# Kernel optimization log

Measured on AMD Instinct MI355X. Metric: run time of the kernel, lower is better.

Reference implementation:

```python
import jax, jax.numpy as jnp
import numpy as np

N_NODES = 100000
N_EDGES = 1600000
D_NODE = 32
D_EDGE = 16
D_HID = 64
D_OUT = 32


def setup_inputs() -> dict:
    key = jax.random.key(0)
    ks = jax.random.split(key, 7)
    x = jax.random.normal(ks[0], (N_NODES, D_NODE), dtype=jnp.float32)
    edge_index = jax.random.randint(ks[1], (2, N_EDGES), 0, N_NODES, dtype=jnp.int64)
    edge_attr = jax.random.normal(ks[2], (N_EDGES, D_EDGE), dtype=jnp.float32)
    # 2-layer MLP params (Linear -> ReLU -> Linear), He-ish scaling
    W1 = jax.random.normal(ks[3], (D_NODE + D_EDGE, D_HID), dtype=jnp.float32) * (2.0 / (D_NODE + D_EDGE)) ** 0.5
    b1 = jnp.zeros((D_HID,), dtype=jnp.float32)
    W2 = jax.random.normal(ks[4], (D_HID, D_OUT), dtype=jnp.float32) * (2.0 / D_HID) ** 0.5
    b2 = jnp.zeros((D_OUT,), dtype=jnp.float32)
    return {"x": x, "edge_index": edge_index, "edge_attr": edge_attr,
            "W1": W1, "b1": b1, "W2": W2, "b2": b2}


def reference(x, edge_index, edge_attr, W1, b1, W2, b2):
    row, col = edge_index[0], edge_index[1]
    # gather source-node feats and concat with edge feats: [E, d_node + d_edge]
    inp = jnp.concatenate([x[col], edge_attr], axis=1)
    # 2-layer MLP over edges
    h = jax.nn.relu(inp @ W1 + b1)
    messages = h @ W2 + b2  # [E, d_out]
    # scatter-sum aggregate by destination node
    message = jax.ops.segment_sum(messages, row, num_segments=x.shape[0])
    return message
```

## Files before the change

### kernel.cpp

```cpp
#include <hip/hip_runtime.h>
#include <hip/hip_bf16.h>
#include <stdint.h>

#define N_NODES 100000
#define N_EDGES 1600000
#define D_NODE  32
#define D_EDGE  16
#define D_IN    48
#define D_HID   64
#define D_OUT   32

#define NFLAGS_OFF  ((size_t)0)
#define NB1_OFF     ((size_t)64)
#define NB2_OFF     ((size_t)320)
#define W1BF_OFF    ((size_t)1024)
#define W2BF_OFF    ((size_t)9216)
#define COUNTS_OFF  ((size_t)65536)
#define OFFSETS_OFF ((size_t)466944)
#define BLKSUM_OFF  ((size_t)917504)
#define RANK_OFF    ((size_t)1048576)
#define MSG_OFF     ((size_t)8388608)

#define SCAN_NB 391

typedef __attribute__((ext_vector_type(8))) short bf16x8;
typedef __attribute__((ext_vector_type(4))) float f32x4;

__device__ inline float bf2f(unsigned int u16) {
    return __uint_as_float(u16 << 16);
}
__device__ inline unsigned short f2bf_rne(float f) {
    unsigned int x = __float_as_uint(f);
    unsigned int r = (x + 0x7FFFu + ((x >> 16) & 1u)) >> 16;
    return (unsigned short)r;
}
__device__ inline unsigned int pk_bf2(float a, float b) {
    float2 f; f.x = a; f.y = b;
    __hip_bfloat162 h = __float22bfloat162_rn(f);
    return *reinterpret_cast<unsigned int*>(&h);
}
__device__ inline float ld_f(const void* p, int i, int isbf) {
    if (isbf) return bf2f(((const unsigned short*)p)[i]);
    return ((const float*)p)[i];
}
__device__ inline bf16x8 pack_bf8(float4 v0, float4 v1) {
    union { unsigned int u[4]; bf16x8 v; } r;
    r.u[0] = pk_bf2(v0.x, v0.y);
    r.u[1] = pk_bf2(v0.z, v0.w);
    r.u[2] = pk_bf2(v1.x, v1.y);
    r.u[3] = pk_bf2(v1.z, v1.w);
    return r.v;
}

__global__ void prep_kernel(const void* __restrict__ xq, const void* __restrict__ idxq,
                            const void* __restrict__ W1q, const void* __restrict__ b1q,
                            const void* __restrict__ W2q, const void* __restrict__ b2q,
                            char* __restrict__ ws) {
    __shared__ int s_isbf;
    const int t = threadIdx.x;
    if (t < 64) {
        unsigned short u = ((const unsigned short*)xq)[t];
        unsigned long long mb = __ballot(((u >> 7) & 0xFF) >= 140);
        int wodd = ((const int*)idxq)[2 * t + 1];
        unsigned long long mi = __ballot(wodd != 0);
        if (t == 0) {
            int* flags = (int*)(ws + NFLAGS_OFF);
            flags[0] = (mb == 0ULL);
            flags[1] = (mi == 0ULL);
            s_isbf = (mb == 0ULL);
        }
    }
    __syncthreads();
    const int isbf = s_isbf;
    float* b1 = (float*)(ws + NB1_OFF);
    float* b2 = (float*)(ws + NB2_OFF);
    unsigned short* w1b = (unsigned short*)(ws + W1BF_OFF);
    unsigned short* w2b = (unsigned short*)(ws + W2BF_OFF);

    if (t < D_HID) b1[t] = ld_f(b1q, t, isbf);
    if (t < D_OUT) b2[t] = ld_f(b2q, t, isbf);

    for (int i = t; i < D_HID * 64; i += blockDim.x) {
        int n = i >> 6, k = i & 63;
        float v = (k < D_IN) ? ld_f(W1q, k * D_HID + n, isbf) : 0.0f;
        w1b[i] = f2bf_rne(v);
    }
    for (int i = t; i < D_OUT * 64; i += blockDim.x) {
        int n = i >> 6, k = i & 63;
        w2b[i] = f2bf_rne(ld_f(W2q, k * D_OUT + n, isbf));
    }
}

__global__ __launch_bounds__(256) void hist_kernel(const void* __restrict__ idxq,
                                                   char* __restrict__ ws,
                                                   int* __restrict__ rankb) {
    const int is64 = ((const int*)(ws + NFLAGS_OFF))[1];
    const int e = blockIdx.x * 256 + threadIdx.x;
    int dst;
    if (is64) dst = (int)((const long long*)idxq)[e];
    else      dst = ((const int*)idxq)[e];
    rankb[e] = atomicAdd((int*)(ws + COUNTS_OFF) + dst, 1);
}

__global__ __launch_bounds__(256) void scan_block_kernel(char* __restrict__ ws) {
    __shared__ int s[256];
    const int* counts = (const int*)(ws + COUNTS_OFF);
    int* offs   = (int*)(ws + OFFSETS_OFF);
    int* blksum = (int*)(ws + BLKSUM_OFF);
    const int t = threadIdx.x;
    const int i = blockIdx.x * 256 + t;
    int v = (i < N_NODES) ? counts[i] : 0;
    s[t] = v;
    __syncthreads();
    for (int d = 1; d < 256; d <<= 1) {
        int a = (t >= d) ? s[t - d] : 0;
        __syncthreads();
        s[t] += a;
        __syncthreads();
    }
    if (i < N_NODES) offs[i] = s[t] - v;
    if (t == 255) blksum[blockIdx.x] = s[255];
}

__global__ __launch_bounds__(256) void scan_add_kernel(char* __restrict__ ws) {
    __shared__ int s[256];
    int* offs = (int*)(ws + OFFSETS_OFF);
    const int* blksum = (const int*)(ws + BLKSUM_OFF);
    const int t = threadIdx.x;
    const int b = blockIdx.x;
    int acc = 0;
    for (int j = t; j < b; j += 256) acc += blksum[j];
    s[t] = acc;
    __syncthreads();
    for (int d = 128; d > 0; d >>= 1) {
        if (t < d) s[t] += s[t + d];
        __syncthreads();
    }
    const int prefix = s[0];
    const int i = b * 256 + t;
    if (i < N_NODES) offs[i] += prefix;
    if (i == 0) offs[N_NODES] = N_EDGES;
}

__global__ __launch_bounds__(64) void edge_mlp_mfma_kernel(
        const void* __restrict__ xq,
        const void* __restrict__ idxq,
        const void* __restrict__ eaq,
        const char* __restrict__ wsro,
        const int* __restrict__ rankb,
        unsigned short* __restrict__ msg) {
    const int isbf = ((const int*)(wsro + NFLAGS_OFF))[0];
    const int is64 = ((const int*)(wsro + NFLAGS_OFF))[1];

    __shared__ __align__(16) unsigned short hbuf[2][16][72];

    const int l   = threadIdx.x;
    const int m16 = l & 15;
    const int q   = l >> 4;

    const unsigned short* w1b = (const unsigned short*)(wsro + W1BF_OFF);
    const unsigned short* w2b = (const unsigned short*)(wsro + W2BF_OFF);
    const float* b1 = (const float*)(wsro + NB1_OFF);
    const float* b2 = (const float*)(wsro + NB2_OFF);
    const int* offs = (const int*)(wsro + OFFSETS_OFF);

    bf16x8 w1f[4][2], w2f[2][2];
#pragma unroll
    for (int t = 0; t < 4; ++t)
#pragma unroll
        for (int c = 0; c < 2; ++c)
            w1f[t][c] = *(const bf16x8*)(w1b + ((t * 16 + m16) * 64 + c * 32 + q * 8));
#pragma unroll
    for (int t = 0; t < 2; ++t)
#pragma unroll
        for (int c = 0; c < 2; ++c)
            w2f[t][c] = *(const bf16x8*)(w2b + ((t * 16 + m16) * 64 + c * 32 + q * 8));

    const int eb = blockIdx.x * 64;

    int srcv[4], posv[4];
#pragma unroll
    for (int g = 0; g < 4; ++g) {
        const int e = eb + g * 16 + m16;
        int dst;
        if (is64) {
            const long long* ip = (const long long*)idxq;
            dst = (int)ip[e];
            srcv[g] = (int)ip[N_EDGES + e];
        } else {
            const int* ip = (const int*)idxq;
            dst = ip[e];
            srcv[g] = ip[N_EDGES + e];
        }
        posv[g] = offs[dst] + rankb[e];
    }

    bf16x8 A0[4], A1[4];
#pragma unroll
    for (int g = 0; g < 4; ++g) {
        const int e = eb + g * 16 + m16;
#pragma unroll
        for (int i = 0; i < 8; ++i) A1[g][i] = 0;
        if (isbf) {
            const unsigned short* x  = (const unsigned short*)xq;
            const unsigned short* ea = (const unsigned short*)eaq;
            A0[g] = *(const bf16x8*)(x + (size_t)srcv[g] * D_NODE + q * 8);
            if (q < 2) A1[g] = *(const bf16x8*)(ea + (size_t)e * D_EDGE + q * 8);
        } else {
            const float* x  = (const float*)xq;
            const float* ea = (const float*)eaq;
            const float4* xp = (const float4*)(x + (size_t)srcv[g] * D_NODE + q * 8);
            A0[g] = pack_bf8(xp[0], xp[1]);
            if (q < 2) {
                const float4* ap = (const float4*)(ea + (size_t)e * D_EDGE + q * 8);
                A1[g] = pack_bf8(ap[0], ap[1]);
            }
        }
    }

    const float b1v[4] = { b1[m16], b1[16 + m16], b1[32 + m16], b1[48 + m16] };
    const float b2v[2] = { b2[m16], b2[16 + m16] };
    const int mrow = l >> 2;
    const int sub  = l & 3;

    auto L1 = [&](int g, int b) {
#pragma unroll
        for (int t = 0; t < 4; ++t) {
            f32x4 c;
            c[0] = c[1] = c[2] = c[3] = b1v[t];
            c = __builtin_amdgcn_mfma_f32_16x16x32_bf16(A0[g], w1f[t][0], c, 0, 0, 0);
            c = __builtin_amdgcn_mfma_f32_16x16x32_bf16(A1[g], w1f[t][1], c, 0, 0, 0);
            unsigned int u0 = pk_bf2(fmaxf(c[0], 0.0f), fmaxf(c[1], 0.0f));
            unsigned int u1 = pk_bf2(fmaxf(c[2], 0.0f), fmaxf(c[3], 0.0f));
            hbuf[b][q * 4 + 0][t * 16 + m16] = (unsigned short)u0;
            hbuf[b][q * 4 + 1][t * 16 + m16] = (unsigned short)(u0 >> 16);
            hbuf[b][q * 4 + 2][t * 16 + m16] = (unsigned short)u1;
            hbuf[b][q * 4 + 3][t * 16 + m16] = (unsigned short)(u1 >> 16);
        }
    };
    auto L2S = [&](int g, int b) {
        bf16x8 a20 = *(const bf16x8*)(&hbuf[b][m16][q * 8]);
        bf16x8 a21 = *(const bf16x8*)(&hbuf[b][m16][32 + q * 8]);
#pragma unroll
        for (int t = 0; t < 2; ++t) {
            f32x4 c;
            c[0] = c[1] = c[2] = c[3] = b2v[t];
            c = __builtin_amdgcn_mfma_f32_16x16x32_bf16(a20, w2f[t][0], c, 0, 0, 0);
            c = __builtin_amdgcn_mfma_f32_16x16x32_bf16(a21, w2f[t][1], c, 0, 0, 0);
            unsigned int u0 = pk_bf2(c[0], c[1]);
            unsigned int u1 = pk_bf2(c[2], c[3]);
            hbuf[b][q * 4 + 0][t * 16 + m16] = (unsigned short)u0;
            hbuf[b][q * 4 + 1][t * 16 + m16] = (unsigned short)(u0 >> 16);
            hbuf[b][q * 4 + 2][t * 16 + m16] = (unsigned short)u1;
            hbuf[b][q * 4 + 3][t * 16 + m16] = (unsigned short)(u1 >> 16);
        }
        const int posm = __shfl(posv[g], mrow, 64);
        uint4 rowv = *(const uint4*)(&hbuf[b][mrow][sub * 8]);
        *(uint4*)(msg + (size_t)posm * D_OUT + sub * 8) = rowv;
    };

    L1(0, 0);
    L1(1, 1);
    L2S(0, 0);
    L1(2, 0);
    L2S(1, 1);
    L1(3, 1);
    L2S(2, 0);
    L2S(3, 1);
}

__global__ __launch_bounds__(256) void reduce_kernel(
        const char* __restrict__ wsro, const unsigned short* __restrict__ msg,
        void* __restrict__ out) {
    const int isbf = ((const int*)(wsro + NFLAGS_OFF))[0];
    const int* offs = (const int*)(wsro + OFFSETS_OFF);
    const int t = blockIdx.x * 256 + threadIdx.x;
    const int node = t >> 4;
    if (node >= N_NODES) return;
    const int c2 = t & 15;
    const int lo = offs[node], hi = offs[node + 1];
    float s0 = 0.0f, s1 = 0.0f;
    const unsigned int* p = (const unsigned int*)msg + (size_t)lo * 16 + c2;
    int k = lo;
    for (; k + 1 < hi; k += 2) {
        unsigned int a = p[0], b = p[16];
        s0 += __uint_as_float(a << 16) + __uint_as_float(b << 16);
        s1 += __uint_as_float(a & 0xFFFF0000u) + __uint_as_float(b & 0xFFFF0000u);
        p += 32;
    }
    if (k < hi) {
        unsigned int a = p[0];
        s0 += __uint_as_float(a << 16);
        s1 += __uint_as_float(a & 0xFFFF0000u);
    }
    if (isbf) {
        ((unsigned int*)out)[(size_t)node * 16 + c2] = pk_bf2(s0, s1);
    } else {
        float2 v; v.x = s0; v.y = s1;
        ((float2*)out)[(size_t)node * 16 + c2] = v;
    }
}

extern "C" void kernel_launch(void* const* d_in, const int* in_sizes, int n_in,
                              void* d_out, int out_size, void* d_ws, size_t ws_size,
                              hipStream_t stream) {
    const void* x   = d_in[0];
    const void* idx = d_in[1];
    const void* ea  = d_in[2];
    const void* W1  = d_in[3];
    const void* b1  = d_in[4];
    const void* W2  = d_in[5];
    const void* b2  = d_in[6];
    char* ws = (char*)d_ws;

    hipMemsetAsync(ws + COUNTS_OFF, 0, (size_t)N_NODES * 4, stream);

    hipLaunchKernelGGL(prep_kernel, dim3(1), dim3(256), 0, stream,
                       x, idx, W1, b1, W2, b2, ws);

    hipLaunchKernelGGL(hist_kernel, dim3(N_EDGES / 256), dim3(256), 0, stream,
                       idx, ws, (int*)(ws + RANK_OFF));

    hipLaunchKernelGGL(scan_block_kernel, dim3(SCAN_NB), dim3(256), 0, stream, ws);
    hipLaunchKernelGGL(scan_add_kernel,   dim3(SCAN_NB), dim3(256), 0, stream, ws);

    hipLaunchKernelGGL(edge_mlp_mfma_kernel, dim3(N_EDGES / 64), dim3(64), 0, stream,
                       x, idx, ea, (const char*)ws,
                       (const int*)(ws + RANK_OFF), (unsigned short*)(ws + MSG_OFF));

    hipLaunchKernelGGL(reduce_kernel, dim3((N_NODES * 16 + 255) / 256), dim3(256), 0, stream,
                       (const char*)ws, (const unsigned short*)(ws + MSG_OFF), d_out);
}
```

Baseline: 380.8 us.

## Fuse count-zeroing into prep kernel and pack four waves per MLP block

Removes the separate memset by having the prep kernel launch many blocks that zero the histogram counts, with block 0 still doing the weight conversion. The edge MLP kernel now runs four independent waves per 256-thread block, each with its own LDS buffer, to cut block count and scheduling overhead. Edge-attribute loads become unconditional, with the upper lane quarters reading duplicate data, which removes the branch and zero-fill. These changes alter the launch structure in three places, and the duplicate edge loads add some redundant memory traffic.

Measured after the change: 369.4 us. -3.0%, faster.

```diff
diff --git a/kernel.cpp b/kernel.cpp
--- a/kernel.cpp
+++ b/kernel.cpp
@@ -52,12 +52,18 @@
     return r.v;
 }
 
-__global__ void prep_kernel(const void* __restrict__ xq, const void* __restrict__ idxq,
-                            const void* __restrict__ W1q, const void* __restrict__ b1q,
-                            const void* __restrict__ W2q, const void* __restrict__ b2q,
-                            char* __restrict__ ws) {
+__global__ __launch_bounds__(256) void prep_kernel(
+        const void* __restrict__ xq, const void* __restrict__ idxq,
+        const void* __restrict__ W1q, const void* __restrict__ b1q,
+        const void* __restrict__ W2q, const void* __restrict__ b2q,
+        char* __restrict__ ws) {
+    const int t = threadIdx.x;
+    const int i0 = blockIdx.x * 256 + t;
+    int* counts = (int*)(ws + COUNTS_OFF);
+    if (i0 < N_NODES) counts[i0] = 0;
+    if (blockIdx.x != 0) return;
+
     __shared__ int s_isbf;
-    const int t = threadIdx.x;
     if (t < 64) {
         unsigned short u = ((const unsigned short*)xq)[t];
         unsigned long long mb = __ballot(((u >> 7) & 0xFF) >= 140);
@@ -80,12 +86,12 @@
     if (t < D_HID) b1[t] = ld_f(b1q, t, isbf);
     if (t < D_OUT) b2[t] = ld_f(b2q, t, isbf);
 
-    for (int i = t; i < D_HID * 64; i += blockDim.x) {
+    for (int i = t; i < D_HID * 64; i += 256) {
         int n = i >> 6, k = i & 63;
         float v = (k < D_IN) ? ld_f(W1q, k * D_HID + n, isbf) : 0.0f;
         w1b[i] = f2bf_rne(v);
     }
-    for (int i = t; i < D_OUT * 64; i += blockDim.x) {
+    for (int i = t; i < D_OUT * 64; i += 256) {
         int n = i >> 6, k = i & 63;
         w2b[i] = f2bf_rne(ld_f(W2q, k * D_OUT + n, isbf));
     }
@@ -142,7 +148,7 @@
     if (i == 0) offs[N_NODES] = N_EDGES;
 }
 
-__global__ __launch_bounds__(64) void edge_mlp_mfma_kernel(
+__global__ __launch_bounds__(256) void edge_mlp_mfma_kernel(
         const void* __restrict__ xq,
         const void* __restrict__ idxq,
         const void* __restrict__ eaq,
@@ -152,9 +158,10 @@
     const int isbf = ((const int*)(wsro + NFLAGS_OFF))[0];
     const int is64 = ((const int*)(wsro + NFLAGS_OFF))[1];
 
-    __shared__ __align__(16) unsigned short hbuf[2][16][72];
-
-    const int l   = threadIdx.x;
+    __shared__ __align__(16) unsigned short hbuf[4][2][16][72];
+
+    const int w   = threadIdx.x >> 6;
+    const int l   = threadIdx.x & 63;
     const int m16 = l & 15;
     const int q   = l >> 4;
 
@@ -176,7 +183,7 @@
         for (int c = 0; c < 2; ++c)
             w2f[t][c] = *(const bf16x8*)(w2b + ((t * 16 + m16) * 64 + c * 32 + q * 8));
 
-    const int eb = blockIdx.x * 64;
+    const int eb = blockIdx.x * 256 + w * 64;
 
     int srcv[4], posv[4];
 #pragma unroll
@@ -199,22 +206,18 @@
 #pragma unroll
     for (int g = 0; g < 4; ++g) {
         const int e = eb + g * 16 + m16;
-#pragma unroll
-        for (int i = 0; i < 8; ++i) A1[g][i] = 0;
         if (isbf) {
             const unsigned short* x  = (const unsigned short*)xq;
             const unsigned short* ea = (const unsigned short*)eaq;
             A0[g] = *(const bf16x8*)(x + (size_t)srcv[g] * D_NODE + q * 8);
-            if (q < 2) A1[g] = *(const bf16x8*)(ea + (size_t)e * D_EDGE + q * 8);
+            A1[g] = *(const bf16x8*)(ea + (size_t)e * D_EDGE + (q & 1) * 8);
         } else {
             const float* x  = (const float*)xq;
             const float* ea = (const float*)eaq;
             const float4* xp = (const float4*)(x + (size_t)srcv[g] * D_NODE + q * 8);
             A0[g] = pack_bf8(xp[0], xp[1]);
-            if (q < 2) {
-                const float4* ap = (const float4*)(ea + (size_t)e * D_EDGE + q * 8);
-                A1[g] = pack_bf8(ap[0], ap[1]);
-            }
+            const float4* ap = (const float4*)(ea + (size_t)e * D_EDGE + (q & 1) * 8);
+            A1[g] = pack_bf8(ap[0], ap[1]);
         }
     }
 
@@ -232,15 +235,15 @@
             c = __builtin_amdgcn_mfma_f32_16x16x32_bf16(A1[g], w1f[t][1], c, 0, 0, 0);
             unsigned int u0 = pk_bf2(fmaxf(c[0], 0.0f), fmaxf(c[1], 0.0f));
             unsigned int u1 = pk_bf2(fmaxf(c[2], 0.0f), fmaxf(c[3], 0.0f));
-            hbuf[b][q * 4 + 0][t * 16 + m16] = (unsigned short)u0;
-            hbuf[b][q * 4 + 1][t * 16 + m16] = (unsigned short)(u0 >> 16);
-            hbuf[b][q * 4 + 2][t * 16 + m16] = (unsigned short)u1;
-            hbuf[b][q * 4 + 3][t * 16 + m16] = (unsigned short)(u1 >> 16);
+            hbuf[w][b][q * 4 + 0][t * 16 + m16] = (unsigned short)u0;
+            hbuf[w][b][q * 4 + 1][t * 16 + m16] = (unsigned short)(u0 >> 16);
+            hbuf[w][b][q * 4 + 2][t * 16 + m16] = (unsigned short)u1;
+            hbuf[w][b][q * 4 + 3][t * 16 + m16] = (unsigned short)(u1 >> 16);
         }
     };
     auto L2S = [&](int g, int b) {
-        bf16x8 a20 = *(const bf16x8*)(&hbuf[b][m16][q * 8]);
-        bf16x8 a21 = *(const bf16x8*)(&hbuf[b][m16][32 + q * 8]);
+        bf16x8 a20 = *(const bf16x8*)(&hbuf[w][b][m16][q * 8]);
+        bf16x8 a21 = *(const bf16x8*)(&hbuf[w][b][m16][32 + q * 8]);
 #pragma unroll
         for (int t = 0; t < 2; ++t) {
             f32x4 c;
@@ -249,13 +252,13 @@
             c = __builtin_amdgcn_mfma_f32_16x16x32_bf16(a21, w2f[t][1], c, 0, 0, 0);
             unsigned int u0 = pk_bf2(c[0], c[1]);
             unsigned int u1 = pk_bf2(c[2], c[3]);
-            hbuf[b][q * 4 + 0][t * 16 + m16] = (unsigned short)u0;
-            hbuf[b][q * 4 + 1][t * 16 + m16] = (unsigned short)(u0 >> 16);
-            hbuf[b][q * 4 + 2][t * 16 + m16] = (unsigned short)u1;
-            hbuf[b][q * 4 + 3][t * 16 + m16] = (unsigned short)(u1 >> 16);
+            hbuf[w][b][q * 4 + 0][t * 16 + m16] = (unsigned short)u0;
+            hbuf[w][b][q * 4 + 1][t * 16 + m16] = (unsigned short)(u0 >> 16);
+            hbuf[w][b][q * 4 + 2][t * 16 + m16] = (unsigned short)u1;
+            hbuf[w][b][q * 4 + 3][t * 16 + m16] = (unsigned short)(u1 >> 16);
         }
         const int posm = __shfl(posv[g], mrow, 64);
-        uint4 rowv = *(const uint4*)(&hbuf[b][mrow][sub * 8]);
+        uint4 rowv = *(const uint4*)(&hbuf[w][b][mrow][sub * 8]);
         *(uint4*)(msg + (size_t)posm * D_OUT + sub * 8) = rowv;
     };
 
@@ -313,9 +316,7 @@
     const void* b2  = d_in[6];
     char* ws = (char*)d_ws;
 
-    hipMemsetAsync(ws + COUNTS_OFF, 0, (size_t)N_NODES * 4, stream);
-
-    hipLaunchKernelGGL(prep_kernel, dim3(1), dim3(256), 0, stream,
+    hipLaunchKernelGGL(prep_kernel, dim3(SCAN_NB), dim3(256), 0, stream,
                        x, idx, W1, b1, W2, b2, ws);
 
     hipLaunchKernelGGL(hist_kernel, dim3(N_EDGES / 256), dim3(256), 0, stream,
@@ -324,7 +325,7 @@
     hipLaunchKernelGGL(scan_block_kernel, dim3(SCAN_NB), dim3(256), 0, stream, ws);
     hipLaunchKernelGGL(scan_add_kernel,   dim3(SCAN_NB), dim3(256), 0, stream, ws);
 
-    hipLaunchKernelGGL(edge_mlp_mfma_kernel, dim3(N_EDGES / 64), dim3(64), 0, stream,
+    hipLaunchKernelGGL(edge_mlp_mfma_kernel, dim3(N_EDGES / 256), dim3(256), 0, stream,
                        x, idx, ea, (const char*)ws,
                        (const int*)(ws + RANK_OFF), (unsigned short*)(ws + MSG_OFF));
 
```
